# Kernel tuning notes

Hardware: AMD Instinct MI355X
Metric: run time of the kernel (lower is better)

The kernel has to match this reference:

```python
import jax, jax.numpy as jnp
import numpy as np

EPS = 1e-5  # torch BatchNorm1d default eps


def _project(x, w1, gamma, beta, w2):
    # Linear(bias=False) -> BatchNorm1d (train mode: batch stats, biased var) -> ReLU -> Linear(bias=False)
    h = x @ w1                                   # (n, 128)
    mu = jnp.mean(h, axis=0)
    var = jnp.var(h, axis=0)                     # biased, as torch uses for normalization
    h = (h - mu) * jax.lax.rsqrt(var + EPS) * gamma + beta
    h = jax.nn.relu(h)
    return h @ w2                                # (n, 128)


def setup_inputs() -> dict:
    key = jax.random.key(0)
    k1, k2, k3, k4 = jax.random.split(key, 4)
    latent, hidden = 512, 128
    n_x, n_y = 8192, 2048
    return {
        "variations": jax.random.normal(k1, (n_x, latent), dtype=jnp.float32),
        "exemplar": jax.random.normal(k2, (n_y, latent), dtype=jnp.float32),
        "w1": jax.random.normal(k3, (latent, hidden), dtype=jnp.float32) * (1.0 / np.sqrt(latent)),
        "gamma": jnp.ones((hidden,), dtype=jnp.float32),
        "beta": jnp.zeros((hidden,), dtype=jnp.float32),
        "w2": jax.random.normal(k4, (hidden, hidden), dtype=jnp.float32) * (1.0 / np.sqrt(hidden)),
    }


def reference(variations, exemplar, w1, gamma, beta, w2):
    z1 = _project(variations, w1, gamma, beta, w2)   # (n_x, d)
    z2 = _project(exemplar, w1, gamma, beta, w2)     # (n_y, d)
    # avoids the (n_x, n_y, d) broadcast intermediate of the original)
    x2 = jnp.sum(z1 * z1, axis=1)[:, None]           # (n_x, 1)
    y2 = jnp.sum(z2 * z2, axis=1)[None, :]           # (1, n_y)
    return x2 + y2 - 2.0 * (z1 @ z2.T)               # (n_x, n_y)
```

## Files before the change

kernel.cpp:

```cpp
#include <hip/hip_runtime.h>
#include <hip/hip_bf16.h>


#define LAT 512
#define HID 128
#define EPSV 1e-5f

typedef __attribute__((ext_vector_type(8))) short bf16x8;
typedef __attribute__((ext_vector_type(4))) float f32x4;

__device__ __forceinline__ unsigned short f2bf(float x) {
  unsigned int u = __builtin_bit_cast(unsigned int, x);
  return (unsigned short)((u + 0x7fffu + ((u >> 16) & 1u)) >> 16);
}
__device__ __forceinline__ float bf2f(unsigned short h) {
  unsigned int u = ((unsigned int)h) << 16;
  return __builtin_bit_cast(float, u);
}
__device__ __forceinline__ size_t pack4_off(int strip, int f, int l15, int lq) {
  return (size_t)strip * 2048 + (size_t)(f >> 1) * 512 + (size_t)l15 * 32 +
         (size_t)(((f & 1) * 2 + (lq >> 1)) * 8 + (lq & 1) * 4);
}

__global__ __launch_bounds__(256) void k_prep(const float* __restrict__ W1,
                                              const float* __restrict__ W2,
                                              const float* __restrict__ X1,
                                              const float* __restrict__ X2, int nx,
                                              unsigned short* __restrict__ W1P,
                                              unsigned short* __restrict__ W2T,
                                              unsigned short* __restrict__ XbP) {
  __shared__ float T[64][65];
  const int t = threadIdx.x;
  int bi = blockIdx.x;
  if (bi >= 20) {
    const size_t base = (size_t)(bi - 20) * 2048 + (size_t)t * 8;
    const size_t nxe = (size_t)nx * LAT;
    const float* src = (base < nxe) ? (X1 + base) : (X2 + (base - nxe));
    const float4 a = *(const float4*)src;
    const float4 b = *(const float4*)(src + 4);
    const int row = (int)(base >> 9);
    const int k = (int)(base & 511);
    const int st = row >> 4, l15 = row & 15;
    const int tf = k >> 5, lq = (k >> 3) & 3;
    const size_t off = ((((size_t)st * 16 + tf) * 16 + l15) * 4 + lq) * 8;
    const ushort4 o0 = {f2bf(a.x), f2bf(a.y), f2bf(a.z), f2bf(a.w)};
    const ushort4 o1 = {f2bf(b.x), f2bf(b.y), f2bf(b.z), f2bf(b.w)};
    *(ushort4*)(XbP + off) = o0;
    *(ushort4*)(XbP + off + 4) = o1;
    return;
  }
  if (bi < 16) {
    const int tk = bi >> 1, tn = bi & 1;
    const int k0 = tk * 64, n0 = tn * 64;
    {
      const int rr = t >> 4, cc = (t & 15) * 4;
#pragma unroll
      for (int i = 0; i < 4; ++i) {
        const int r = rr + i * 16;
        const float4 v = *(const float4*)(W1 + (size_t)(k0 + r) * HID + n0 + cc);
        T[cc + 0][r] = v.x; T[cc + 1][r] = v.y; T[cc + 2][r] = v.z; T[cc + 3][r] = v.w;
      }
    }
    __syncthreads();
    {
      const int nn = t >> 2, q = (t & 3) * 16;
      const int n = n0 + nn;
      const int f = n >> 4, l15 = n & 15;
#pragma unroll
      for (int e8 = 0; e8 < 2; ++e8) {
        const int kq = q + e8 * 8;
        const int kk = k0 + kq;
        const int tf = kk >> 5, lq = (kk >> 3) & 3;
        const size_t off = ((((size_t)f * 16 + tf) * 16 + l15) * 4 + lq) * 8;
        const ushort4 lo = {f2bf(T[nn][kq + 0]), f2bf(T[nn][kq + 1]),
                            f2bf(T[nn][kq + 2]), f2bf(T[nn][kq + 3])};
        const ushort4 hi = {f2bf(T[nn][kq + 4]), f2bf(T[nn][kq + 5]),
                            f2bf(T[nn][kq + 6]), f2bf(T[nn][kq + 7])};
        *(ushort4*)(W1P + off) = lo;
        *(ushort4*)(W1P + off + 4) = hi;
      }
    }
  } else {
    bi -= 16;
    const int tk = bi >> 1, tn = bi & 1;
    const int k0 = tk * 64, n0 = tn * 64;
    {
      const int rr = t >> 4, cc = (t & 15) * 4;
#pragma unroll
      for (int i = 0; i < 4; ++i) {
        const int r = rr + i * 16;
        const float4 v = *(const float4*)(W2 + (size_t)(k0 + r) * HID + n0 + cc);
        T[cc + 0][r] = v.x; T[cc + 1][r] = v.y; T[cc + 2][r] = v.z; T[cc + 3][r] = v.w;
      }
    }
    __syncthreads();
    {
      const int nn = t >> 2, q = (t & 3) * 16;
      unsigned short* dp = W2T + (size_t)(n0 + nn) * HID + k0 + q;
#pragma unroll
      for (int j = 0; j < 4; ++j) {
        ushort4 o = {f2bf(T[nn][q + j * 4 + 0]), f2bf(T[nn][q + j * 4 + 1]),
                     f2bf(T[nn][q + j * 4 + 2]), f2bf(T[nn][q + j * 4 + 3])};
        *(ushort4*)(dp + j * 4) = o;
      }
    }
  }
}

__global__ __launch_bounds__(256) void k_gemm1(
    const unsigned short* __restrict__ XbP,
    const unsigned short* __restrict__ W1P, unsigned short* __restrict__ H,
    float* __restrict__ pS, float* __restrict__ pQ) {
  __shared__ float sS[16][HID], sQ[16][HID];
  const int tid = threadIdx.x, wid = tid >> 6, lane = tid & 63;
  const int l15 = lane & 15, lq = lane >> 4;
  const int row0 = (int)blockIdx.x * 64 + wid * 16;
  const int strip = row0 >> 4;
  const unsigned short* xp = XbP + (((size_t)strip * 16 * 16 + l15) * 4 + lq) * 8;
  const unsigned short* wp = W1P + (((size_t)l15) * 4 + lq) * 8;
  f32x4 acc[8];
#pragma unroll
  for (int f = 0; f < 8; ++f) acc[f] = (f32x4){0.f, 0.f, 0.f, 0.f};

#pragma unroll
  for (int t = 0; t < 16; ++t) {
    const bf16x8 xv = *(const bf16x8*)(xp + (size_t)t * 512);
#pragma unroll
    for (int f = 0; f < 8; ++f) {
      const bf16x8 afr = *(const bf16x8*)(wp + (size_t)(f * 16 + t) * 512);
      acc[f] = __builtin_amdgcn_mfma_f32_16x16x32_bf16(afr, xv, acc[f], 0, 0, 0);
    }
  }
#pragma unroll
  for (int f = 0; f < 8; ++f) {
    ushort4 hz = {f2bf(acc[f][0]), f2bf(acc[f][1]), f2bf(acc[f][2]), f2bf(acc[f][3])};
    *(ushort4*)(H + pack4_off(strip, f, l15, lq)) = hz;
  }
#pragma unroll
  for (int f = 0; f < 8; ++f) {
    f32x4 s = acc[f];
    f32x4 q = acc[f] * acc[f];
#pragma unroll
    for (int r = 0; r < 4; ++r) {
      s[r] += __shfl_xor(s[r], 1, 64);
      q[r] += __shfl_xor(q[r], 1, 64);
      s[r] += __shfl_xor(s[r], 2, 64);
      q[r] += __shfl_xor(q[r], 2, 64);
    }
    if ((l15 & 3) == 0) {
      *(f32x4*)&sS[wid * 4 + (l15 >> 2)][f * 16 + lq * 4] = s;
      *(f32x4*)&sQ[wid * 4 + (l15 >> 2)][f * 16 + lq * 4] = q;
    }
  }
  __syncthreads();
  if (tid < HID) {
    float s = 0.f, q = 0.f;
#pragma unroll
    for (int r = 0; r < 16; ++r) { s += sS[r][tid]; q += sQ[r][tid]; }
    pS[(size_t)blockIdx.x * HID + tid] = s;
    pQ[(size_t)blockIdx.x * HID + tid] = q;
  }
}

__global__ __launch_bounds__(256) void k_gemm2(
    const unsigned short* __restrict__ H,
    const unsigned short* __restrict__ W2T,
    const float* __restrict__ pS, const float* __restrict__ pQ,
    const float* __restrict__ gamma, const float* __restrict__ beta,
    unsigned short* __restrict__ Z, float* __restrict__ nrm,
    int nb1, int nblk, float n1c, float n2c) {
  __shared__ float s_sc[HID], s_sh[HID];
  __shared__ float t0[2][HID], t1[2][HID];
  const int tid = threadIdx.x, wid = tid >> 6, lane = tid & 63;
  const int l15 = lane & 15, lq = lane >> 4, lk8 = lq * 8;
  const bool set1 = (int)blockIdx.x < nb1;
  {
    const int col = tid & 127, half = tid >> 7;
    const int b0 = set1 ? 0 : nb1;
    const int nb = set1 ? nb1 : (nblk - nb1);
    float s = 0.f, q = 0.f;
#pragma unroll 4
    for (int b = half; b < nb; b += 2) {
      s += pS[(size_t)(b0 + b) * HID + col];
      q += pQ[(size_t)(b0 + b) * HID + col];
    }
    t0[half][col] = s;
    t1[half][col] = q;
  }
  __syncthreads();
  if (tid < HID) {
    const float s = t0[0][tid] + t0[1][tid];
    const float q = t1[0][tid] + t1[1][tid];
    const float n = set1 ? n1c : n2c;
    const float mean = s / n;
    const float var = q / n - mean * mean;
    const float rstd = rsqrtf(var + EPSV);
    const float scale = gamma[tid] * rstd;
    s_sc[tid] = scale;
    s_sh[tid] = beta[tid] - mean * scale;
  }
  __syncthreads();
  const int row0 = (int)blockIdx.x * 64 + wid * 16;
  const int strip = row0 >> 4;
  const unsigned short* hptr = H + (size_t)strip * 2048 + (size_t)l15 * 32 + lk8;
  f32x4 acc[8];
#pragma unroll
  for (int f = 0; f < 8; ++f) acc[f] = (f32x4){0.f, 0.f, 0.f, 0.f};
#pragma unroll
  for (int s = 0; s < 4; ++s) {
    const int k = s * 32 + lk8;
    const bf16x8 hv = *(const bf16x8*)(hptr + (size_t)s * 512);
    const float4 c0 = *(const float4*)&s_sc[k];
    const float4 c1 = *(const float4*)&s_sc[k + 4];
    const float4 d0 = *(const float4*)&s_sh[k];
    const float4 d1 = *(const float4*)&s_sh[k + 4];
    const float cc[8] = {c0.x, c0.y, c0.z, c0.w, c1.x, c1.y, c1.z, c1.w};
    const float dd[8] = {d0.x, d0.y, d0.z, d0.w, d1.x, d1.y, d1.z, d1.w};
    bf16x8 bfr;
#pragma unroll
    for (int i = 0; i < 8; ++i) {
      const float a = fmaxf(fmaf(bf2f((unsigned short)hv[i]), cc[i], dd[i]), 0.f);
      bfr[i] = (short)f2bf(a);
    }
#pragma unroll
    for (int f = 0; f < 8; ++f) {
      const bf16x8 afr = *(const bf16x8*)(W2T + (size_t)(f * 16 + l15) * HID + k);
      acc[f] = __builtin_amdgcn_mfma_f32_16x16x32_bf16(afr, bfr, acc[f], 0, 0, 0);
    }
  }
  float rn = 0.f;
#pragma unroll
  for (int f = 0; f < 8; ++f) {
    rn += acc[f][0] * acc[f][0] + acc[f][1] * acc[f][1] +
          acc[f][2] * acc[f][2] + acc[f][3] * acc[f][3];
    ushort4 z4 = {f2bf(acc[f][0]), f2bf(acc[f][1]), f2bf(acc[f][2]), f2bf(acc[f][3])};
    *(ushort4*)(Z + pack4_off(strip, f, l15, lq)) = z4;
  }
  rn += __shfl_xor(rn, 16, 64);
  rn += __shfl_xor(rn, 32, 64);
  if (lane < 16) nrm[row0 + l15] = rn;
}

__global__ __launch_bounds__(256) void k_dist(const unsigned short* __restrict__ Z1b,
                                              const unsigned short* __restrict__ Z2b,
                                              const float* __restrict__ n1,
                                              const float* __restrict__ n2,
                                              float* __restrict__ D, int NY, int ntx) {
  const int nwg = (int)gridDim.x;
  const int cpx = nwg >> 3;
  const int bid = (int)blockIdx.x;
  const int wgid = (bid & 7) * cpx + (bid >> 3);
  const int tby = wgid / ntx, tbx = wgid - tby * ntx;

  const int tid = threadIdx.x;
  const int wid = tid >> 6, lane = tid & 63;
  const int wr = wid >> 1, wc = wid & 1;
  const int rowB = tby * 128 + wr * 64;
  const int colB = tbx * 128 + wc * 64;
  const int l15 = lane & 15, lq = lane >> 4;
  const unsigned short* Ap = Z1b + (size_t)(rowB >> 4) * 2048 + (size_t)l15 * 32 + lq * 8;
  const unsigned short* Bp = Z2b + (size_t)(colB >> 4) * 2048 + (size_t)l15 * 32 + lq * 8;
  f32x4 acc[4][4];
#pragma unroll
  for (int i = 0; i < 4; ++i)
#pragma unroll
    for (int j = 0; j < 4; ++j) acc[i][j] = (f32x4){0.f, 0.f, 0.f, 0.f};
#pragma unroll
  for (int s = 0; s < 4; ++s) {
    bf16x8 a[4], b[4];
#pragma unroll
    for (int i = 0; i < 4; ++i) a[i] = *(const bf16x8*)(Ap + (size_t)i * 2048 + (size_t)s * 512);
#pragma unroll
    for (int j = 0; j < 4; ++j) b[j] = *(const bf16x8*)(Bp + (size_t)j * 2048 + (size_t)s * 512);
#pragma unroll
    for (int i = 0; i < 4; ++i)
#pragma unroll
      for (int j = 0; j < 4; ++j)
        acc[i][j] = __builtin_amdgcn_mfma_f32_16x16x32_bf16(b[j], a[i], acc[i][j], 0, 0, 0);
  }
  const int cq = lq * 4;
  float na[4];
#pragma unroll
  for (int i = 0; i < 4; ++i) na[i] = n1[rowB + i * 16 + l15];
#pragma unroll
  for (int j = 0; j < 4; ++j) {
    const float4 nbv = *(const float4*)(n2 + colB + j * 16 + cq);
#pragma unroll
    for (int i = 0; i < 4; ++i) {
      float4 o;
      o.x = na[i] + nbv.x - 2.f * acc[i][j][0];
      o.y = na[i] + nbv.y - 2.f * acc[i][j][1];
      o.z = na[i] + nbv.z - 2.f * acc[i][j][2];
      o.w = na[i] + nbv.w - 2.f * acc[i][j][3];
      *(float4*)(D + (size_t)(rowB + i * 16 + l15) * NY + colB + j * 16 + cq) = o;
    }
  }
}

extern "C" void kernel_launch(void* const* d_in, const int* in_sizes, int n_in,
                              void* d_out, int out_size, void* d_ws, size_t ws_size,
                              hipStream_t stream) {
  const float* variations = (const float*)d_in[0];
  const float* exemplar   = (const float*)d_in[1];
  const float* w1         = (const float*)d_in[2];
  const float* gamma      = (const float*)d_in[3];
  const float* beta       = (const float*)d_in[4];
  const float* w2         = (const float*)d_in[5];
  float* D = (float*)d_out;

  const int nx = in_sizes[0] / LAT;
  const int ny = in_sizes[1] / LAT;
  const int nrows = nx + ny;
  const int nbb = nrows / 64;
  const int nb1 = nx / 64;

  char* p = (char*)d_ws;
  unsigned short* XbP = (unsigned short*)p; p += (size_t)nrows * LAT * 2;
  unsigned short* Hb  = (unsigned short*)p; p += (size_t)nrows * HID * 2;
  unsigned short* Zb  = (unsigned short*)p; p += (size_t)nrows * HID * 2;
  unsigned short* W1P = (unsigned short*)p; p += (size_t)LAT * HID * 2;
  unsigned short* W2T = (unsigned short*)p; p += (size_t)HID * HID * 2;
  float* pS = (float*)p;  p += (size_t)nbb * HID * 4;
  float* pQ = (float*)p;  p += (size_t)nbb * HID * 4;
  float* nrmAll = (float*)p; p += (size_t)nrows * 4;
  float* n1v = nrmAll;
  float* n2v = nrmAll + nx;
  unsigned short* Z1b = Zb;
  unsigned short* Z2b = Zb + (size_t)nx * HID;

  const int xblocks = (nrows * LAT) / 2048;
  k_prep<<<20 + xblocks, 256, 0, stream>>>(w1, w2, variations, exemplar, nx,
                                           W1P, W2T, XbP);
  k_gemm1<<<nbb, 256, 0, stream>>>(XbP, W1P, Hb, pS, pQ);
  k_gemm2<<<nbb, 256, 0, stream>>>(Hb, W2T, pS, pQ, gamma, beta, Zb, nrmAll,
                                   nb1, nbb, (float)nx, (float)ny);
  const int ntx = ny / 128;
  const int nwg = (nx / 128) * ntx;
  k_dist<<<nwg, 256, 0, stream>>>(Z1b, Z2b, n1v, n2v, D, ny, ntx);
}
```

Baseline: 58.81 us.

## Fuse weight and input bf16 conversion into GEMM kernels and drop prep kernel

Removes the separate prep kernel. Each k_gemm1 block now converts all of W1 into a packed bf16 layout in about 144 KB of dynamic LDS, then reads the fp32 activations straight from global memory and converts them in registers. k_gemm2 likewise builds its bf16 W2 tile in LDS instead of reading a pre-transposed global copy. This saves a launch and the round trip of the bf16 activation copy through global memory. In exchange, every block redundantly converts the weights behind many serial barriers, and the large LDS footprint limits gemm1 to one block per CU.

```diff
diff --git a/kernel.cpp b/kernel.cpp
--- a/kernel.cpp
+++ b/kernel.cpp
@@ -5,6 +5,7 @@
 #define LAT 512
 #define HID 128
 #define EPSV 1e-5f
+#define G1_LDS (131072 + 16640)
 
 typedef __attribute__((ext_vector_type(8))) short bf16x8;
 typedef __attribute__((ext_vector_type(4))) float f32x4;
@@ -22,115 +23,80 @@
          (size_t)(((f & 1) * 2 + (lq >> 1)) * 8 + (lq & 1) * 4);
 }
 
-__global__ __launch_bounds__(256) void k_prep(const float* __restrict__ W1,
-                                              const float* __restrict__ W2,
-                                              const float* __restrict__ X1,
-                                              const float* __restrict__ X2, int nx,
-                                              unsigned short* __restrict__ W1P,
-                                              unsigned short* __restrict__ W2T,
-                                              unsigned short* __restrict__ XbP) {
-  __shared__ float T[64][65];
-  const int t = threadIdx.x;
-  int bi = blockIdx.x;
-  if (bi >= 20) {
-    const size_t base = (size_t)(bi - 20) * 2048 + (size_t)t * 8;
-    const size_t nxe = (size_t)nx * LAT;
-    const float* src = (base < nxe) ? (X1 + base) : (X2 + (base - nxe));
-    const float4 a = *(const float4*)src;
-    const float4 b = *(const float4*)(src + 4);
-    const int row = (int)(base >> 9);
-    const int k = (int)(base & 511);
-    const int st = row >> 4, l15 = row & 15;
-    const int tf = k >> 5, lq = (k >> 3) & 3;
-    const size_t off = ((((size_t)st * 16 + tf) * 16 + l15) * 4 + lq) * 8;
-    const ushort4 o0 = {f2bf(a.x), f2bf(a.y), f2bf(a.z), f2bf(a.w)};
-    const ushort4 o1 = {f2bf(b.x), f2bf(b.y), f2bf(b.z), f2bf(b.w)};
-    *(ushort4*)(XbP + off) = o0;
-    *(ushort4*)(XbP + off + 4) = o1;
-    return;
-  }
-  if (bi < 16) {
-    const int tk = bi >> 1, tn = bi & 1;
-    const int k0 = tk * 64, n0 = tn * 64;
-    {
-      const int rr = t >> 4, cc = (t & 15) * 4;
-#pragma unroll
-      for (int i = 0; i < 4; ++i) {
-        const int r = rr + i * 16;
-        const float4 v = *(const float4*)(W1 + (size_t)(k0 + r) * HID + n0 + cc);
-        T[cc + 0][r] = v.x; T[cc + 1][r] = v.y; T[cc + 2][r] = v.z; T[cc + 3][r] = v.w;
-      }
-    }
-    __syncthreads();
-    {
-      const int nn = t >> 2, q = (t & 3) * 16;
-      const int n = n0 + nn;
-      const int f = n >> 4, l15 = n & 15;
-#pragma unroll
-      for (int e8 = 0; e8 < 2; ++e8) {
-        const int kq = q + e8 * 8;
-        const int kk = k0 + kq;
-        const int tf = kk >> 5, lq = (kk >> 3) & 3;
-        const size_t off = ((((size_t)f * 16 + tf) * 16 + l15) * 4 + lq) * 8;
-        const ushort4 lo = {f2bf(T[nn][kq + 0]), f2bf(T[nn][kq + 1]),
-                            f2bf(T[nn][kq + 2]), f2bf(T[nn][kq + 3])};
-        const ushort4 hi = {f2bf(T[nn][kq + 4]), f2bf(T[nn][kq + 5]),
-                            f2bf(T[nn][kq + 6]), f2bf(T[nn][kq + 7])};
-        *(ushort4*)(W1P + off) = lo;
-        *(ushort4*)(W1P + off + 4) = hi;
-      }
-    }
-  } else {
-    bi -= 16;
-    const int tk = bi >> 1, tn = bi & 1;
-    const int k0 = tk * 64, n0 = tn * 64;
-    {
-      const int rr = t >> 4, cc = (t & 15) * 4;
-#pragma unroll
-      for (int i = 0; i < 4; ++i) {
-        const int r = rr + i * 16;
-        const float4 v = *(const float4*)(W2 + (size_t)(k0 + r) * HID + n0 + cc);
-        T[cc + 0][r] = v.x; T[cc + 1][r] = v.y; T[cc + 2][r] = v.z; T[cc + 3][r] = v.w;
-      }
-    }
-    __syncthreads();
-    {
-      const int nn = t >> 2, q = (t & 3) * 16;
-      unsigned short* dp = W2T + (size_t)(n0 + nn) * HID + k0 + q;
-#pragma unroll
-      for (int j = 0; j < 4; ++j) {
-        ushort4 o = {f2bf(T[nn][q + j * 4 + 0]), f2bf(T[nn][q + j * 4 + 1]),
-                     f2bf(T[nn][q + j * 4 + 2]), f2bf(T[nn][q + j * 4 + 3])};
-        *(ushort4*)(dp + j * 4) = o;
-      }
-    }
-  }
-}
-
+template <int TPF>
+__device__ __forceinline__ void conv_tile(const float* __restrict__ W, int k0, int n0,
+                                          float (*T)[65], unsigned short* WL, int tid) {
+  {
+    const int rr = tid >> 4, cc = (tid & 15) * 4;
+#pragma unroll
+    for (int i = 0; i < 4; ++i) {
+      const int r = rr + i * 16;
+      const float4 v = *(const float4*)(W + (size_t)(k0 + r) * HID + n0 + cc);
+      T[cc + 0][r] = v.x; T[cc + 1][r] = v.y; T[cc + 2][r] = v.z; T[cc + 3][r] = v.w;
+    }
+  }
+  __syncthreads();
+  {
+    const int nn = tid >> 2, q = (tid & 3) * 16;
+    const int n = n0 + nn, f = n >> 4, nl = n & 15;
+#pragma unroll
+    for (int e8 = 0; e8 < 2; ++e8) {
+      const int k = k0 + q + e8 * 8;
+      const int tt = k >> 5, kq = (k >> 3) & 3;
+      const int kl = q + e8 * 8;
+      ushort4 lo = {f2bf(T[nn][kl + 0]), f2bf(T[nn][kl + 1]),
+                    f2bf(T[nn][kl + 2]), f2bf(T[nn][kl + 3])};
+      ushort4 hi = {f2bf(T[nn][kl + 4]), f2bf(T[nn][kl + 5]),
+                    f2bf(T[nn][kl + 6]), f2bf(T[nn][kl + 7])};
+      char* dst = (char*)WL + (size_t)(f * TPF + tt) * 1024 + kq * 256 + nl * 16;
+      *(ushort4*)dst = lo;
+      *(ushort4*)(dst + 8) = hi;
+    }
+  }
+  __syncthreads();
+}
+
+extern __shared__ char smem_g1[];
 __global__ __launch_bounds__(256) void k_gemm1(
-    const unsigned short* __restrict__ XbP,
-    const unsigned short* __restrict__ W1P, unsigned short* __restrict__ H,
+    const float* __restrict__ X1, const float* __restrict__ X2, int nx,
+    const float* __restrict__ W1, unsigned short* __restrict__ H,
     float* __restrict__ pS, float* __restrict__ pQ) {
-  __shared__ float sS[16][HID], sQ[16][HID];
+  unsigned short* WL = (unsigned short*)smem_g1;
+  char* aux = smem_g1 + 131072;
+  float(*T)[65] = (float(*)[65])aux;
+  float(*sS)[HID] = (float(*)[HID])aux;
+  float(*sQ)[HID] = (float(*)[HID])(aux + 8192);
   const int tid = threadIdx.x, wid = tid >> 6, lane = tid & 63;
   const int l15 = lane & 15, lq = lane >> 4;
-  const int row0 = (int)blockIdx.x * 64 + wid * 16;
+
+#pragma unroll 1
+  for (int bi = 0; bi < 16; ++bi)
+    conv_tile<16>(W1, (bi >> 1) * 64, (bi & 1) * 64, T, WL, tid);
+
+  const int browBase = (int)blockIdx.x * 64;
+  const int row0 = browBase + wid * 16;
+  const float* X = (browBase < nx) ? X1 : X2;
+  const int xrow = (browBase < nx) ? row0 : row0 - nx;
+  const float* xptr = X + (size_t)(xrow + l15) * LAT + lq * 8;
+  const char* wl = (const char*)WL + lq * 256 + l15 * 16;
+  f32x4 acc[8];
+#pragma unroll
+  for (int f = 0; f < 8; ++f) acc[f] = (f32x4){0.f, 0.f, 0.f, 0.f};
+#pragma unroll
+  for (int t = 0; t < 16; ++t) {
+    const float4 x0 = *(const float4*)(xptr + t * 32);
+    const float4 x1 = *(const float4*)(xptr + t * 32 + 4);
+    const float vv[8] = {x0.x, x0.y, x0.z, x0.w, x1.x, x1.y, x1.z, x1.w};
+    bf16x8 xv;
+#pragma unroll
+    for (int i = 0; i < 8; ++i) xv[i] = (short)f2bf(vv[i]);
+#pragma unroll
+    for (int f = 0; f < 8; ++f) {
+      const bf16x8 afr = *(const bf16x8*)(wl + (size_t)(f * 16 + t) * 1024);
+      acc[f] = __builtin_amdgcn_mfma_f32_16x16x32_bf16(afr, xv, acc[f], 0, 0, 0);
+    }
+  }
   const int strip = row0 >> 4;
-  const unsigned short* xp = XbP + (((size_t)strip * 16 * 16 + l15) * 4 + lq) * 8;
-  const unsigned short* wp = W1P + (((size_t)l15) * 4 + lq) * 8;
-  f32x4 acc[8];
-#pragma unroll
-  for (int f = 0; f < 8; ++f) acc[f] = (f32x4){0.f, 0.f, 0.f, 0.f};
-
-#pragma unroll
-  for (int t = 0; t < 16; ++t) {
-    const bf16x8 xv = *(const bf16x8*)(xp + (size_t)t * 512);
-#pragma unroll
-    for (int f = 0; f < 8; ++f) {
-      const bf16x8 afr = *(const bf16x8*)(wp + (size_t)(f * 16 + t) * 512);
-      acc[f] = __builtin_amdgcn_mfma_f32_16x16x32_bf16(afr, xv, acc[f], 0, 0, 0);
-    }
-  }
 #pragma unroll
   for (int f = 0; f < 8; ++f) {
     ushort4 hz = {f2bf(acc[f][0]), f2bf(acc[f][1]), f2bf(acc[f][2]), f2bf(acc[f][3])};
@@ -163,18 +129,20 @@
 }
 
 __global__ __launch_bounds__(256) void k_gemm2(
-    const unsigned short* __restrict__ H,
-    const unsigned short* __restrict__ W2T,
+    const unsigned short* __restrict__ H, const float* __restrict__ W2,
     const float* __restrict__ pS, const float* __restrict__ pQ,
     const float* __restrict__ gamma, const float* __restrict__ beta,
     unsigned short* __restrict__ Z, float* __restrict__ nrm,
     int nb1, int nblk, float n1c, float n2c) {
+  __shared__ unsigned short W2L[16384];
+  __shared__ float aux2[64 * 65];
   __shared__ float s_sc[HID], s_sh[HID];
-  __shared__ float t0[2][HID], t1[2][HID];
   const int tid = threadIdx.x, wid = tid >> 6, lane = tid & 63;
   const int l15 = lane & 15, lq = lane >> 4, lk8 = lq * 8;
   const bool set1 = (int)blockIdx.x < nb1;
   {
+    float* t0 = aux2;
+    float* t1 = aux2 + 2 * HID;
     const int col = tid & 127, half = tid >> 7;
     const int b0 = set1 ? 0 : nb1;
     const int nb = set1 ? nb1 : (nblk - nb1);
@@ -184,25 +152,32 @@
       s += pS[(size_t)(b0 + b) * HID + col];
       q += pQ[(size_t)(b0 + b) * HID + col];
     }
-    t0[half][col] = s;
-    t1[half][col] = q;
-  }
-  __syncthreads();
-  if (tid < HID) {
-    const float s = t0[0][tid] + t0[1][tid];
-    const float q = t1[0][tid] + t1[1][tid];
-    const float n = set1 ? n1c : n2c;
-    const float mean = s / n;
-    const float var = q / n - mean * mean;
-    const float rstd = rsqrtf(var + EPSV);
-    const float scale = gamma[tid] * rstd;
-    s_sc[tid] = scale;
-    s_sh[tid] = beta[tid] - mean * scale;
-  }
-  __syncthreads();
+    t0[half * HID + col] = s;
+    t1[half * HID + col] = q;
+    __syncthreads();
+    if (tid < HID) {
+      const float ss = t0[tid] + t0[HID + tid];
+      const float qq = t1[tid] + t1[HID + tid];
+      const float n = set1 ? n1c : n2c;
+      const float mean = ss / n;
+      const float var = qq / n - mean * mean;
+      const float rstd = rsqrtf(var + EPSV);
+      const float scale = gamma[tid] * rstd;
+      s_sc[tid] = scale;
+      s_sh[tid] = beta[tid] - mean * scale;
+    }
+    __syncthreads();
+  }
+  {
+    float(*T)[65] = (float(*)[65])aux2;
+#pragma unroll 1
+    for (int bi = 0; bi < 4; ++bi)
+      conv_tile<4>(W2, (bi >> 1) * 64, (bi & 1) * 64, T, W2L, tid);
+  }
   const int row0 = (int)blockIdx.x * 64 + wid * 16;
   const int strip = row0 >> 4;
   const unsigned short* hptr = H + (size_t)strip * 2048 + (size_t)l15 * 32 + lk8;
+  const char* wl = (const char*)W2L + lq * 256 + l15 * 16;
   f32x4 acc[8];
 #pragma unroll
   for (int f = 0; f < 8; ++f) acc[f] = (f32x4){0.f, 0.f, 0.f, 0.f};
@@ -224,7 +199,7 @@
     }
 #pragma unroll
     for (int f = 0; f < 8; ++f) {
-      const bf16x8 afr = *(const bf16x8*)(W2T + (size_t)(f * 16 + l15) * HID + k);
+      const bf16x8 afr = *(const bf16x8*)(wl + (size_t)(f * 4 + s) * 1024);
       acc[f] = __builtin_amdgcn_mfma_f32_16x16x32_bf16(afr, bfr, acc[f], 0, 0, 0);
     }
   }
@@ -315,11 +290,8 @@
   const int nb1 = nx / 64;
 
   char* p = (char*)d_ws;
-  unsigned short* XbP = (unsigned short*)p; p += (size_t)nrows * LAT * 2;
-  unsigned short* Hb  = (unsigned short*)p; p += (size_t)nrows * HID * 2;
-  unsigned short* Zb  = (unsigned short*)p; p += (size_t)nrows * HID * 2;
-  unsigned short* W1P = (unsigned short*)p; p += (size_t)LAT * HID * 2;
-  unsigned short* W2T = (unsigned short*)p; p += (size_t)HID * HID * 2;
+  unsigned short* Hb = (unsigned short*)p; p += (size_t)nrows * HID * 2;
+  unsigned short* Zb = (unsigned short*)p; p += (size_t)nrows * HID * 2;
   float* pS = (float*)p;  p += (size_t)nbb * HID * 4;
   float* pQ = (float*)p;  p += (size_t)nbb * HID * 4;
   float* nrmAll = (float*)p; p += (size_t)nrows * 4;
@@ -328,11 +300,8 @@
   unsigned short* Z1b = Zb;
   unsigned short* Z2b = Zb + (size_t)nx * HID;
 
-  const int xblocks = (nrows * LAT) / 2048;
-  k_prep<<<20 + xblocks, 256, 0, stream>>>(w1, w2, variations, exemplar, nx,
-                                           W1P, W2T, XbP);
-  k_gemm1<<<nbb, 256, 0, stream>>>(XbP, W1P, Hb, pS, pQ);
-  k_gemm2<<<nbb, 256, 0, stream>>>(Hb, W2T, pS, pQ, gamma, beta, Zb, nrmAll,
+  k_gemm1<<<nbb, 256, G1_LDS, stream>>>(variations, exemplar, nx, w1, Hb, pS, pQ);
+  k_gemm2<<<nbb, 256, 0, stream>>>(Hb, w2, pS, pQ, gamma, beta, Zb, nrmAll,
                                    nb1, nbb, (float)nx, (float)ny);
   const int ntx = ny / 128;
   const int nwg = (nx / 128) * ntx;
```

Measured after the change: 61.64 us. +4.8%, slower.

## Split GEMM1 work per 16-row strip across waves by output column groups

Applied to the files above, without the earlier changes.

Each k_gemm1 block now handles one 16-row strip, and its four waves each compute two of the eight 16-column output fragments, instead of each wave computing all eight fragments for its own strip. This raises the grid from nrows/64 to nrows/16 blocks and cuts per-wave accumulator registers, which should improve occupancy and parallelism. The cost is that the X strip is loaded redundantly by all four waves and there are four times as many partial-stat rows for k_gemm2 to reduce.

```diff
diff --git a/kernel.cpp b/kernel.cpp
--- a/kernel.cpp
+++ b/kernel.cpp
@@ -111,35 +111,32 @@
     const unsigned short* __restrict__ XbP,
     const unsigned short* __restrict__ W1P, unsigned short* __restrict__ H,
     float* __restrict__ pS, float* __restrict__ pQ) {
-  __shared__ float sS[16][HID], sQ[16][HID];
-  const int tid = threadIdx.x, wid = tid >> 6, lane = tid & 63;
+  __shared__ float sS[4][HID], sQ[4][HID];
+  const int tid = threadIdx.x, w = tid >> 6, lane = tid & 63;
   const int l15 = lane & 15, lq = lane >> 4;
-  const int row0 = (int)blockIdx.x * 64 + wid * 16;
-  const int strip = row0 >> 4;
-  const unsigned short* xp = XbP + (((size_t)strip * 16 * 16 + l15) * 4 + lq) * 8;
-  const unsigned short* wp = W1P + (((size_t)l15) * 4 + lq) * 8;
-  f32x4 acc[8];
-#pragma unroll
-  for (int f = 0; f < 8; ++f) acc[f] = (f32x4){0.f, 0.f, 0.f, 0.f};
-
+  const int b = (int)blockIdx.x;
+  const unsigned short* xp = XbP + (size_t)b * 8192 + (size_t)l15 * 32 + lq * 8;
+  const unsigned short* wp = W1P + (size_t)l15 * 32 + lq * 8;
+  f32x4 acc[2];
+  acc[0] = (f32x4){0.f, 0.f, 0.f, 0.f};
+  acc[1] = (f32x4){0.f, 0.f, 0.f, 0.f};
 #pragma unroll
   for (int t = 0; t < 16; ++t) {
     const bf16x8 xv = *(const bf16x8*)(xp + (size_t)t * 512);
 #pragma unroll
-    for (int f = 0; f < 8; ++f) {
+    for (int ff = 0; ff < 2; ++ff) {
+      const int f = w * 2 + ff;
       const bf16x8 afr = *(const bf16x8*)(wp + (size_t)(f * 16 + t) * 512);
-      acc[f] = __builtin_amdgcn_mfma_f32_16x16x32_bf16(afr, xv, acc[f], 0, 0, 0);
-    }
-  }
-#pragma unroll
-  for (int f = 0; f < 8; ++f) {
-    ushort4 hz = {f2bf(acc[f][0]), f2bf(acc[f][1]), f2bf(acc[f][2]), f2bf(acc[f][3])};
-    *(ushort4*)(H + pack4_off(strip, f, l15, lq)) = hz;
-  }
-#pragma unroll
-  for (int f = 0; f < 8; ++f) {
-    f32x4 s = acc[f];
-    f32x4 q = acc[f] * acc[f];
+      acc[ff] = __builtin_amdgcn_mfma_f32_16x16x32_bf16(afr, xv, acc[ff], 0, 0, 0);
+    }
+  }
+#pragma unroll
+  for (int ff = 0; ff < 2; ++ff) {
+    const int f = w * 2 + ff;
+    ushort4 hz = {f2bf(acc[ff][0]), f2bf(acc[ff][1]), f2bf(acc[ff][2]), f2bf(acc[ff][3])};
+    *(ushort4*)(H + pack4_off(b, f, l15, lq)) = hz;
+    f32x4 s = acc[ff];
+    f32x4 q = acc[ff] * acc[ff];
 #pragma unroll
     for (int r = 0; r < 4; ++r) {
       s[r] += __shfl_xor(s[r], 1, 64);
@@ -148,17 +145,16 @@
       q[r] += __shfl_xor(q[r], 2, 64);
     }
     if ((l15 & 3) == 0) {
-      *(f32x4*)&sS[wid * 4 + (l15 >> 2)][f * 16 + lq * 4] = s;
-      *(f32x4*)&sQ[wid * 4 + (l15 >> 2)][f * 16 + lq * 4] = q;
+      *(f32x4*)&sS[l15 >> 2][f * 16 + lq * 4] = s;
+      *(f32x4*)&sQ[l15 >> 2][f * 16 + lq * 4] = q;
     }
   }
   __syncthreads();
   if (tid < HID) {
-    float s = 0.f, q = 0.f;
-#pragma unroll
-    for (int r = 0; r < 16; ++r) { s += sS[r][tid]; q += sQ[r][tid]; }
-    pS[(size_t)blockIdx.x * HID + tid] = s;
-    pQ[(size_t)blockIdx.x * HID + tid] = q;
+    const float s = sS[0][tid] + sS[1][tid] + sS[2][tid] + sS[3][tid];
+    const float q = sQ[0][tid] + sQ[1][tid] + sQ[2][tid] + sQ[3][tid];
+    pS[(size_t)b * HID + tid] = s;
+    pQ[(size_t)b * HID + tid] = q;
   }
 }
 
@@ -168,16 +164,17 @@
     const float* __restrict__ pS, const float* __restrict__ pQ,
     const float* __restrict__ gamma, const float* __restrict__ beta,
     unsigned short* __restrict__ Z, float* __restrict__ nrm,
-    int nb1, int nblk, float n1c, float n2c) {
+    int pb1, int pnblk, float n1c, float n2c, int nx) {
   __shared__ float s_sc[HID], s_sh[HID];
   __shared__ float t0[2][HID], t1[2][HID];
   const int tid = threadIdx.x, wid = tid >> 6, lane = tid & 63;
   const int l15 = lane & 15, lq = lane >> 4, lk8 = lq * 8;
-  const bool set1 = (int)blockIdx.x < nb1;
+  const int row0 = (int)blockIdx.x * 64 + wid * 16;
+  const bool set1 = ((int)blockIdx.x * 64) < nx;
   {
     const int col = tid & 127, half = tid >> 7;
-    const int b0 = set1 ? 0 : nb1;
-    const int nb = set1 ? nb1 : (nblk - nb1);
+    const int b0 = set1 ? 0 : pb1;
+    const int nb = set1 ? pb1 : (pnblk - pb1);
     float s = 0.f, q = 0.f;
 #pragma unroll 4
     for (int b = half; b < nb; b += 2) {
@@ -200,7 +197,6 @@
     s_sh[tid] = beta[tid] - mean * scale;
   }
   __syncthreads();
-  const int row0 = (int)blockIdx.x * 64 + wid * 16;
   const int strip = row0 >> 4;
   const unsigned short* hptr = H + (size_t)strip * 2048 + (size_t)l15 * 32 + lk8;
   f32x4 acc[8];
@@ -311,8 +307,9 @@
   const int nx = in_sizes[0] / LAT;
   const int ny = in_sizes[1] / LAT;
   const int nrows = nx + ny;
+  const int nst = nrows / 16;
+  const int pb1 = nx / 16;
   const int nbb = nrows / 64;
-  const int nb1 = nx / 64;
 
   char* p = (char*)d_ws;
   unsigned short* XbP = (unsigned short*)p; p += (size_t)nrows * LAT * 2;
@@ -320,8 +317,8 @@
   unsigned short* Zb  = (unsigned short*)p; p += (size_t)nrows * HID * 2;
   unsigned short* W1P = (unsigned short*)p; p += (size_t)LAT * HID * 2;
   unsigned short* W2T = (unsigned short*)p; p += (size_t)HID * HID * 2;
-  float* pS = (float*)p;  p += (size_t)nbb * HID * 4;
-  float* pQ = (float*)p;  p += (size_t)nbb * HID * 4;
+  float* pS = (float*)p;  p += (size_t)nst * HID * 4;
+  float* pQ = (float*)p;  p += (size_t)nst * HID * 4;
   float* nrmAll = (float*)p; p += (size_t)nrows * 4;
   float* n1v = nrmAll;
   float* n2v = nrmAll + nx;
@@ -331,9 +328,9 @@
   const int xblocks = (nrows * LAT) / 2048;
   k_prep<<<20 + xblocks, 256, 0, stream>>>(w1, w2, variations, exemplar, nx,
                                            W1P, W2T, XbP);
-  k_gemm1<<<nbb, 256, 0, stream>>>(XbP, W1P, Hb, pS, pQ);
+  k_gemm1<<<nst, 256, 0, stream>>>(XbP, W1P, Hb, pS, pQ);
   k_gemm2<<<nbb, 256, 0, stream>>>(Hb, W2T, pS, pQ, gamma, beta, Zb, nrmAll,
-                                   nb1, nbb, (float)nx, (float)ny);
+                                   pb1, nst, (float)nx, (float)ny, nx);
   const int ntx = ny / 128;
   const int nwg = (nx / 128) * ntx;
   k_dist<<<nwg, 256, 0, stream>>>(Z1b, Z2b, n1v, n2v, D, ny, ntx);
```

Measured after the change: 68.57 us. 16.6% more time.
